# Optimization experiments

Hardware: AMD Instinct MI355X
Metric: run time of the kernel (lower is better)

Reference implementation:

```python
import jax, jax.numpy as jnp
import numpy as np

NUM_HEADS = 16
LORA_RANK = 64
LORA_ALPHA = 1.0


def setup_inputs() -> dict:
    key = jax.random.key(0)
    ks = jax.random.split(key, 9)
    B, N, C, r = 16, 1024, 1024, LORA_RANK
    s = lambda k, shp, sc=0.02: (jax.random.normal(k, shp, dtype=jnp.float32) * sc)
    return {
        "x": jax.random.normal(ks[0], (B, N, C), dtype=jnp.float32),
        "W_qkv": s(ks[1], (3 * C, C)),
        "b_qkv": s(ks[2], (3 * C,)),
        "lora_kA": s(ks[3], (r, C), 1.0 / np.sqrt(r)),
        "lora_kB": s(ks[4], (C, r)),
        "lora_vA": s(ks[5], (r, C), 1.0 / np.sqrt(r)),
        "lora_vB": s(ks[6], (C, r)),
        "W_proj": s(ks[7], (C, C)),
        "b_proj": s(ks[8], (C,)),
    }


def reference(x, W_qkv, b_qkv, lora_kA, lora_kB, lora_vA, lora_vB, W_proj, b_proj):
    B, N, C = x.shape
    H = NUM_HEADS
    D = C // H
    scale = D ** -0.5
    lora_scale = LORA_ALPHA / LORA_RANK

    # qkv projection: (B,N,3C)
    qkv = x @ W_qkv.T + b_qkv
    # LoRA deltas for k and v: x @ A.T @ B.T * (alpha/rank)
    k_lora = ((x @ lora_kA.T) @ lora_kB.T) * lora_scale  # (B,N,C)
    v_lora = ((x @ lora_vA.T) @ lora_vB.T) * lora_scale  # (B,N,C)

    qkv = qkv.reshape(B, N, 3, H, D).transpose(2, 0, 3, 1, 4)  # (3,B,H,N,D)
    q, k, v = qkv[0], qkv[1], qkv[2]
    k = k + k_lora.reshape(B, N, H, D).transpose(0, 2, 1, 3)
    v = v + v_lora.reshape(B, N, H, D).transpose(0, 2, 1, 3)

    attn = jnp.einsum('bhqd,bhkd->bhqk', q, k) * scale  # (B,H,N,N)
    attn = jax.nn.softmax(attn, axis=-1)
    out = jnp.einsum('bhqk,bhkd->bhqd', attn, v)  # (B,H,N,D)
    out = out.transpose(0, 2, 1, 3).reshape(B, N, C)
    return out @ W_proj.T + b_proj
```

## Files before the change

### kernel.cpp

```cpp
#include <hip/hip_runtime.h>
#include <hip/hip_bf16.h>
#include <stdint.h>

#define B_  16
#define N_  1024
#define C_  1024
#define H_  16
#define Dh  64
#define M_  (B_*N_)
#define QSCALE (0.125f * 1.44269504f)

typedef __attribute__((ext_vector_type(8)))  short short8;
typedef __attribute__((ext_vector_type(4)))  float f32x4;
typedef __attribute__((ext_vector_type(16))) float f32x16;

__device__ __forceinline__ ushort f2bf(float f) {
  union { float f; uint32_t u; } v; v.f = f;
  uint32_t u = v.u;
  u += 0x7fffu + ((u >> 16) & 1u);
  return (ushort)(u >> 16);
}

__device__ __forceinline__ ushort f2bf_fast(float f) {
  union { float f; uint32_t u; } v; v.f = f;
  return (ushort)((v.u + 0x8000u) >> 16);
}

__device__ __forceinline__ float exp2fast(float x) {
#if __has_builtin(__builtin_amdgcn_exp2f)
  return __builtin_amdgcn_exp2f(x);
#else
  return exp2f(x);
#endif
}

__device__ __forceinline__ void gload_lds16(const ushort* g, ushort* l) {
  __builtin_amdgcn_global_load_lds((const __attribute__((address_space(1))) void*)g,
                                   (__attribute__((address_space(3))) void*)l, 16, 0, 0);
}

struct CastSegs {
  const float* src[7];
  ushort*      dst[7];
  int          cum[7];
  float        scale[7];
};

__global__ void cast_all_k(CastSegs sg, int total4) {
  int i = blockIdx.x * blockDim.x + threadIdx.x;
  int stride = gridDim.x * blockDim.x;
  for (; i < total4; i += stride) {
    int s = 0;
    #pragma unroll
    for (int k = 0; k < 6; ++k) s += (i >= sg.cum[k]);
    int base = s ? sg.cum[s-1] : 0;
    int li = i - base;
    float sc = sg.scale[s];
    float4 v = reinterpret_cast<const float4*>(sg.src[s])[li];
    ushort4 o;
    o.x = f2bf(v.x * sc);
    o.y = f2bf(v.y * sc);
    o.z = f2bf(v.z * sc);
    o.w = f2bf(v.w * sc);
    reinterpret_cast<ushort4*>(sg.dst[s])[li] = o;
  }
}

template<int MODE>
__global__ __launch_bounds__(256)
void gemm128(const ushort* __restrict__ A, int lda,
             const ushort* __restrict__ Bm, int ldb,
             const float* __restrict__ bias,
             const ushort* __restrict__ A2,
             const ushort* __restrict__ B2k, const ushort* __restrict__ B2v,
             ushort* __restrict__ oq, ushort* __restrict__ ok, ushort* __restrict__ ov,
             float* __restrict__ of, int ldo)
{
  __shared__ ushort sA[2][128*32];
  __shared__ ushort sB[2][128*32];
  const int t = threadIdx.x;
  const int lane = t & 63, w = t >> 6;
  const int wr = w >> 1, wc = w & 1;
  const int r = lane & 15, g = lane >> 4;
  const int m0 = blockIdx.x * 128, n0 = blockIdx.y * 128;

  const int s = n0 >> 10;
  int nt = 32;
  const ushort* A2b = nullptr; const ushort* B2 = nullptr; int n0loc = 0;
  if (MODE == 1 && s == 1) {
    nt = 34;
    A2b = A2;
    B2 = B2k;
    n0loc = n0 - 1024;
  }
  if (MODE == 3) nt = 34;

  auto stage = [&](int buf, int tt) {
    const ushort* Ab; const ushort* Bb; int ldaT, ldbT;
    if (tt < 32) { Ab = A + m0*lda + tt*32; ldaT = lda; Bb = Bm + n0*ldb + tt*32; ldbT = ldb; }
    else if (MODE == 3) {
      Ab = A2 + m0*64 + (tt-32)*32; ldaT = 64;
      Bb = B2k + n0*128 + (tt-32)*32; ldbT = 128;
    } else {
      Ab = A2b + m0*128 + (tt-32)*32; ldaT = 128;
      Bb = B2 + n0loc*64 + (tt-32)*32; ldbT = 64;
    }
    #pragma unroll
    for (int i = 0; i < 2; ++i) {
      int c = i*256 + t;
      gload_lds16(Ab + (c>>2)*ldaT + (c&3)*8, &sA[buf][c*8]);
      gload_lds16(Bb + (c>>2)*ldbT + (c&3)*8, &sB[buf][c*8]);
    }
  };

  f32x4 acc[4][4];
  #pragma unroll
  for (int i=0;i<4;++i)
    #pragma unroll
    for (int j=0;j<4;++j) acc[i][j] = (f32x4){0.f,0.f,0.f,0.f};

  stage(0, 0);
  __syncthreads();
  for (int tt = 0; tt < nt; ++tt) {
    int cur = tt & 1;
    if (tt + 1 < nt) stage(cur ^ 1, tt + 1);
    short8 af[4], bfr[4];
    #pragma unroll
    for (int i=0;i<4;++i) af[i]  = *(const short8*)&sA[cur][(wr*64 + i*16 + r)*32 + g*8];
    #pragma unroll
    for (int j=0;j<4;++j) bfr[j] = *(const short8*)&sB[cur][(wc*64 + j*16 + r)*32 + g*8];
    #pragma unroll
    for (int i=0;i<4;++i)
      #pragma unroll
      for (int j=0;j<4;++j)
        acc[i][j] = __builtin_amdgcn_mfma_f32_16x16x32_bf16(af[i], bfr[j], acc[i][j], 0,0,0);
    __syncthreads();
  }

  #pragma unroll
  for (int i=0;i<4;++i) {
    #pragma unroll
    for (int j=0;j<4;++j) {
      #pragma unroll
      for (int rr=0;rr<4;++rr) {
        int m = m0 + wr*64 + i*16 + g*4 + rr;
        int n = n0 + wc*64 + j*16 + r;
        float v = acc[i][j][rr];
        if (MODE == 0) {
          oq[m*128 + n] = f2bf(v);
        } else if (MODE == 1) {
          v += bias[n];
          int b = m >> 10, nq = m & 1023;
          int c = n & 1023, h = c >> 6, d = c & 63;
          int idx = ((b*H_ + h)*N_ + nq)*Dh + d;
          if (s == 0)      oq[idx] = f2bf(v * QSCALE);
          else             ok[idx] = f2bf(v);
        } else if (MODE == 3) {
          v += bias[m];
          int h = m >> 6, d = m & 63;
          int b = n >> 10, nq = n & 1023;
          ov[((b*H_ + h)*Dh + d)*N_ + nq] = f2bf(v);
        } else {
          of[m*ldo + n] = v + bias[n];
        }
      }
    }
  }
}

__global__ __launch_bounds__(512)
void flash_attn32(const ushort* __restrict__ qb, const ushort* __restrict__ kb,
                  const ushort* __restrict__ vb, ushort* __restrict__ out)
{
  __shared__ ushort Kt[2][64*64];
  __shared__ ushort Vt[2][64*64];
  const int t = threadIdx.x, w = t >> 6, lane = t & 63;
  const int ql = lane & 31, hi = lane >> 5;

  int bid = (blockIdx.x & 7) * 128 + (blockIdx.x >> 3);
  const int bh = bid >> 2, qt = bid & 3;
  const int b = bh >> 4, h = bh & 15;
  const ushort* Q  = qb + bh * (N_*Dh);
  const ushort* K  = kb + bh * (N_*Dh);
  const ushort* VT = vb + bh * (Dh*N_);
  const int q0 = qt*256 + w*32;

  short8 qf[4];
  #pragma unroll
  for (int ds=0; ds<4; ++ds)
    qf[ds] = *(const short8*)&Q[(q0 + ql)*Dh + ds*16 + hi*8];

  short8 ones;
  #pragma unroll
  for (int j=0;j<8;++j) ones[j] = (short)0x3F80;

  f32x16 o0, o1, lacc;
  #pragma unroll
  for (int r=0;r<16;++r) { o0[r]=0.f; o1[r]=0.f; lacc[r]=0.f; }
  float m = -1e30f;

  const int srow = t >> 3, scc = (t & 7) ^ ((t >> 3) & 7);
  const ushort* Ksrc = K  + srow*Dh + scc*8;
  const ushort* Vsrc = VT + srow*N_ + scc*8;
  ushort* Kdst = &Kt[0][t*8];
  ushort* Vdst = &Vt[0][t*8];

  const int krA = ql, krB = 32 + ql;
  const int kbaseA = krA*64, kbaseB = krB*64, kmA = krA & 7, kmB = krB & 7;

  auto stage = [&](int buf, int kt) {
    gload_lds16(Ksrc + kt*(64*Dh), Kdst + buf*(64*64));
    gload_lds16(Vsrc + kt*64,      Vdst + buf*(64*64));
  };

  stage(0, 0);

  for (int kt = 0; kt < 16; ++kt) {
    int cur = kt & 1;
    asm volatile("s_waitcnt vmcnt(0)" ::: "memory");
    __builtin_amdgcn_sched_barrier(0);
    __builtin_amdgcn_s_barrier();
    if (kt < 15) stage(cur ^ 1, kt + 1);

    const ushort* Kl = &Kt[cur][0];
    const ushort* Vl = &Vt[cur][0];

    f32x16 s0, s1;
    #pragma unroll
    for (int r=0;r<16;++r) { s0[r]=0.f; s1[r]=0.f; }
    __builtin_amdgcn_s_setprio(1);
    #pragma unroll
    for (int ds=0; ds<4; ++ds) {
      int sc0 = ds*2 + hi;
      short8 kfA = *(const short8*)&Kl[kbaseA + ((sc0 ^ kmA)*8)];
      short8 kfB = *(const short8*)&Kl[kbaseB + ((sc0 ^ kmB)*8)];
      s0 = __builtin_amdgcn_mfma_f32_32x32x16_bf16(kfA, qf[ds], s0, 0,0,0);
      s1 = __builtin_amdgcn_mfma_f32_32x32x16_bf16(kfB, qf[ds], s1, 0,0,0);
    }
    __builtin_amdgcn_s_setprio(0);

    float pm = -1e30f;
    #pragma unroll
    for (int r=0;r<16;++r) pm = fmaxf(pm, fmaxf(s0[r], s1[r]));
    pm = fmaxf(pm, __shfl_xor(pm, 32));

    if (__any(pm > m + 8.f)) {
      float nm = fmaxf(m, pm);
      float fac = exp2fast(m - nm);
      m = nm;
      #pragma unroll
      for (int r=0;r<16;++r) {
        int qr = (r&3) + 8*(r>>2) + 4*hi;
        float facr = __shfl(fac, qr);
        o0[r] *= facr; o1[r] *= facr; lacc[r] *= facr;
      }
    }

    #pragma unroll
    for (int sg=0; sg<4; ++sg) {
      const int rb = (sg & 1) * 8;
      float e0,e1,e2,e3,e4,e5,e6,e7;
      if (sg < 2) {
        e0=exp2fast(s0[rb+0]-m); e1=exp2fast(s0[rb+1]-m);
        e2=exp2fast(s0[rb+2]-m); e3=exp2fast(s0[rb+3]-m);
        e4=exp2fast(s0[rb+4]-m); e5=exp2fast(s0[rb+5]-m);
        e6=exp2fast(s0[rb+6]-m); e7=exp2fast(s0[rb+7]-m);
      } else {
        e0=exp2fast(s1[rb+0]-m); e1=exp2fast(s1[rb+1]-m);
        e2=exp2fast(s1[rb+2]-m); e3=exp2fast(s1[rb+3]-m);
        e4=exp2fast(s1[rb+4]-m); e5=exp2fast(s1[rb+5]-m);
        e6=exp2fast(s1[rb+6]-m); e7=exp2fast(s1[rb+7]-m);
      }
      uint32_t w01 = (uint32_t)f2bf_fast(e0) | ((uint32_t)f2bf_fast(e1) << 16);
      uint32_t w23 = (uint32_t)f2bf_fast(e2) | ((uint32_t)f2bf_fast(e3) << 16);
      uint32_t w45 = (uint32_t)f2bf_fast(e4) | ((uint32_t)f2bf_fast(e5) << 16);
      uint32_t w67 = (uint32_t)f2bf_fast(e6) | ((uint32_t)f2bf_fast(e7) << 16);
      uint32_t x01 = __shfl_xor(w01, 32);
      uint32_t x23 = __shfl_xor(w23, 32);
      uint32_t x45 = __shfl_xor(w45, 32);
      uint32_t x67 = __shfl_xor(w67, 32);
      union { uint32_t u[4]; short8 s8; } pu;
      pu.u[0] = hi ? x45 : w01;
      pu.u[1] = hi ? x67 : w23;
      pu.u[2] = hi ? w45 : x01;
      pu.u[3] = hi ? w67 : x23;
      short8 pf = pu.s8;

      int sc0 = sg*2 + hi;
      short8 vfA = *(const short8*)&Vl[kbaseA + ((sc0 ^ kmA)*8)];
      short8 vfB = *(const short8*)&Vl[kbaseB + ((sc0 ^ kmB)*8)];
      __builtin_amdgcn_s_setprio(1);
      o0   = __builtin_amdgcn_mfma_f32_32x32x16_bf16(pf, vfA, o0, 0,0,0);
      o1   = __builtin_amdgcn_mfma_f32_32x32x16_bf16(pf, vfB, o1, 0,0,0);
      lacc = __builtin_amdgcn_mfma_f32_32x32x16_bf16(pf, ones, lacc, 0,0,0);
      __builtin_amdgcn_s_setprio(0);
    }
  }

  #pragma unroll
  for (int r=0;r<16;++r) {
    float inv = 1.f / lacc[r];
    int qr = (r&3) + 8*(r>>2) + 4*hi;
    int row = b*N_ + q0 + qr;
    out[row*C_ + h*Dh + ql]      = f2bf(o0[r] * inv);
    out[row*C_ + h*Dh + 32 + ql] = f2bf(o1[r] * inv);
  }
}

extern "C" void kernel_launch(void* const* d_in, const int* in_sizes, int n_in,
                              void* d_out, int out_size, void* d_ws, size_t ws_size,
                              hipStream_t stream)
{
  const float* x      = (const float*)d_in[0];
  const float* W_qkv  = (const float*)d_in[1];
  const float* b_qkv  = (const float*)d_in[2];
  const float* kA     = (const float*)d_in[3];
  const float* kB     = (const float*)d_in[4];
  const float* vA     = (const float*)d_in[5];
  const float* vB     = (const float*)d_in[6];
  const float* W_proj = (const float*)d_in[7];
  const float* b_proj = (const float*)d_in[8];
  float* out = (float*)d_out;

  ushort* ws    = (ushort*)d_ws;
  ushort* xb    = ws;
  ushort* wqkvb = xb + 16777216;
  ushort* kvAb  = wqkvb + 3145728;
  ushort* kBb   = kvAb + 131072;
  ushort* vBb   = kBb + 65536;
  ushort* wprojb= vBb + 65536;
  ushort* tkv   = wprojb + 1048576;
  ushort* qbuf  = tkv + 2097152;
  ushort* kbuf  = qbuf + 16777216;
  ushort* vbuf  = kbuf + 16777216;
  ushort* attn  = xb;

  const float ls = 1.0f / 64.0f;

  CastSegs sg;
  const float* srcs[7] = { x, W_qkv, kA, vA, kB, vB, W_proj };
  ushort* dsts[7]      = { xb, wqkvb, kvAb, kvAb + 65536, kBb, vBb, wprojb };
  int     n4s[7]       = { 16777216/4, 3145728/4, 65536/4, 65536/4, 65536/4, 65536/4, 1048576/4 };
  float   scs[7]       = { 1.f, 1.f, 1.f, 1.f, ls, ls, 1.f };
  int cum = 0;
  for (int i = 0; i < 7; ++i) {
    sg.src[i] = srcs[i]; sg.dst[i] = dsts[i]; sg.scale[i] = scs[i];
    cum += n4s[i]; sg.cum[i] = cum;
  }
  cast_all_k<<<dim3(4096), dim3(256), 0, stream>>>(sg, cum);

  gemm128<0><<<dim3(128, 1), dim3(256), 0, stream>>>(
      xb, 1024, kvAb, 1024, nullptr, nullptr, nullptr, nullptr,
      tkv, nullptr, nullptr, nullptr, 0);

  gemm128<1><<<dim3(128, 16), dim3(256), 0, stream>>>(
      xb, 1024, wqkvb, 1024, b_qkv, tkv, kBb, nullptr,
      qbuf, kbuf, nullptr, nullptr, 0);

  gemm128<3><<<dim3(8, 128), dim3(256), 0, stream>>>(
      wqkvb + 2048*1024, 1024, xb, 1024, b_qkv + 2048, vBb, tkv + 64, nullptr,
      nullptr, nullptr, vbuf, nullptr, 0);

  flash_attn32<<<dim3(1024), dim3(512), 0, stream>>>(qbuf, kbuf, vbuf, attn);

  gemm128<2><<<dim3(128, 8), dim3(256), 0, stream>>>(
      attn, 1024, wprojb, 1024, b_proj, nullptr, nullptr, nullptr,
      nullptr, nullptr, nullptr, out, 1024);
}
```

Measured before the change: 394.0 us.

## Drop ones-MFMA row-sum in flash attention and use 256-thread blocks

Replaces the extra MFMA against a ones vector, which accumulated the softmax denominator, with a scalar fp32 running sum of the exponentials that is combined across half-waves at the end. This removes one of three MFMAs in the PV loop along with a 16-register accumulator. The attention kernel also moves from 512-thread to 256-thread blocks (2048 blocks, 128 queries each, launch_bounds 256,4), with each thread staging two K/V chunks per tile. The row max is computed as a tree reduction. Smaller blocks raise occupancy and shorten barriers, but each block reloads K/V tiles for fewer queries, doubling K/V traffic.

```diff
diff --git a/kernel.cpp b/kernel.cpp
--- a/kernel.cpp
+++ b/kernel.cpp
@@ -168,7 +168,7 @@
   }
 }
 
-__global__ __launch_bounds__(512)
+__global__ __launch_bounds__(256, 4)
 void flash_attn32(const ushort* __restrict__ qb, const ushort* __restrict__ kb,
                   const ushort* __restrict__ vb, ushort* __restrict__ out)
 {
@@ -177,40 +177,41 @@
   const int t = threadIdx.x, w = t >> 6, lane = t & 63;
   const int ql = lane & 31, hi = lane >> 5;
 
-  int bid = (blockIdx.x & 7) * 128 + (blockIdx.x >> 3);
-  const int bh = bid >> 2, qt = bid & 3;
+  int bid = (blockIdx.x & 7) * 256 + (blockIdx.x >> 3);
+  const int bh = bid >> 3, qt = bid & 7;
   const int b = bh >> 4, h = bh & 15;
   const ushort* Q  = qb + bh * (N_*Dh);
   const ushort* K  = kb + bh * (N_*Dh);
   const ushort* VT = vb + bh * (Dh*N_);
-  const int q0 = qt*256 + w*32;
+  const int q0 = qt*128 + w*32;
 
   short8 qf[4];
   #pragma unroll
   for (int ds=0; ds<4; ++ds)
     qf[ds] = *(const short8*)&Q[(q0 + ql)*Dh + ds*16 + hi*8];
 
-  short8 ones;
-  #pragma unroll
-  for (int j=0;j<8;++j) ones[j] = (short)0x3F80;
-
-  f32x16 o0, o1, lacc;
-  #pragma unroll
-  for (int r=0;r<16;++r) { o0[r]=0.f; o1[r]=0.f; lacc[r]=0.f; }
+  f32x16 o0, o1;
+  #pragma unroll
+  for (int r=0;r<16;++r) { o0[r]=0.f; o1[r]=0.f; }
+  float lsum = 0.f;
   float m = -1e30f;
 
   const int srow = t >> 3, scc = (t & 7) ^ ((t >> 3) & 7);
-  const ushort* Ksrc = K  + srow*Dh + scc*8;
-  const ushort* Vsrc = VT + srow*N_ + scc*8;
+  const ushort* Ksrc0 = K  + srow*Dh + scc*8;
+  const ushort* Vsrc0 = VT + srow*N_ + scc*8;
   ushort* Kdst = &Kt[0][t*8];
   ushort* Vdst = &Vt[0][t*8];
 
-  const int krA = ql, krB = 32 + ql;
-  const int kbaseA = krA*64, kbaseB = krB*64, kmA = krA & 7, kmB = krB & 7;
+  const int kbaseA = ql*64, kbaseB = (32 + ql)*64;
+  const int kmA = ql & 7, kmB = kmA;
 
   auto stage = [&](int buf, int kt) {
-    gload_lds16(Ksrc + kt*(64*Dh), Kdst + buf*(64*64));
-    gload_lds16(Vsrc + kt*64,      Vdst + buf*(64*64));
+    const ushort* Kp = Ksrc0 + kt*(64*Dh);
+    const ushort* Vp = Vsrc0 + kt*64;
+    gload_lds16(Kp,          Kdst + buf*4096);
+    gload_lds16(Kp + 32*Dh,  Kdst + buf*4096 + 2048);
+    gload_lds16(Vp,          Vdst + buf*4096);
+    gload_lds16(Vp + 32*N_,  Vdst + buf*4096 + 2048);
   };
 
   stage(0, 0);
@@ -239,20 +240,25 @@
     }
     __builtin_amdgcn_s_setprio(0);
 
-    float pm = -1e30f;
-    #pragma unroll
-    for (int r=0;r<16;++r) pm = fmaxf(pm, fmaxf(s0[r], s1[r]));
+    float tm[8];
+    #pragma unroll
+    for (int i=0;i<8;++i)
+      tm[i] = fmaxf(fmaxf(s0[i], s0[i+8]), fmaxf(s1[i], s1[i+8]));
+    float ta = fmaxf(fmaxf(tm[0],tm[1]), fmaxf(tm[2],tm[3]));
+    float tb = fmaxf(fmaxf(tm[4],tm[5]), fmaxf(tm[6],tm[7]));
+    float pm = fmaxf(ta, tb);
     pm = fmaxf(pm, __shfl_xor(pm, 32));
 
     if (__any(pm > m + 8.f)) {
       float nm = fmaxf(m, pm);
       float fac = exp2fast(m - nm);
       m = nm;
+      lsum *= fac;
       #pragma unroll
       for (int r=0;r<16;++r) {
         int qr = (r&3) + 8*(r>>2) + 4*hi;
         float facr = __shfl(fac, qr);
-        o0[r] *= facr; o1[r] *= facr; lacc[r] *= facr;
+        o0[r] *= facr; o1[r] *= facr;
       }
     }
 
@@ -271,6 +277,7 @@
         e4=exp2fast(s1[rb+4]-m); e5=exp2fast(s1[rb+5]-m);
         e6=exp2fast(s1[rb+6]-m); e7=exp2fast(s1[rb+7]-m);
       }
+      lsum += ((e0+e1)+(e2+e3)) + ((e4+e5)+(e6+e7));
       uint32_t w01 = (uint32_t)f2bf_fast(e0) | ((uint32_t)f2bf_fast(e1) << 16);
       uint32_t w23 = (uint32_t)f2bf_fast(e2) | ((uint32_t)f2bf_fast(e3) << 16);
       uint32_t w45 = (uint32_t)f2bf_fast(e4) | ((uint32_t)f2bf_fast(e5) << 16);
@@ -290,20 +297,21 @@
       short8 vfA = *(const short8*)&Vl[kbaseA + ((sc0 ^ kmA)*8)];
       short8 vfB = *(const short8*)&Vl[kbaseB + ((sc0 ^ kmB)*8)];
       __builtin_amdgcn_s_setprio(1);
-      o0   = __builtin_amdgcn_mfma_f32_32x32x16_bf16(pf, vfA, o0, 0,0,0);
-      o1   = __builtin_amdgcn_mfma_f32_32x32x16_bf16(pf, vfB, o1, 0,0,0);
-      lacc = __builtin_amdgcn_mfma_f32_32x32x16_bf16(pf, ones, lacc, 0,0,0);
+      o0 = __builtin_amdgcn_mfma_f32_32x32x16_bf16(pf, vfA, o0, 0,0,0);
+      o1 = __builtin_amdgcn_mfma_f32_32x32x16_bf16(pf, vfB, o1, 0,0,0);
       __builtin_amdgcn_s_setprio(0);
     }
   }
 
+  float lfull = lsum + __shfl_xor(lsum, 32);
+  float inv = 1.f / lfull;
   #pragma unroll
   for (int r=0;r<16;++r) {
-    float inv = 1.f / lacc[r];
     int qr = (r&3) + 8*(r>>2) + 4*hi;
+    float invr = __shfl(inv, qr);
     int row = b*N_ + q0 + qr;
-    out[row*C_ + h*Dh + ql]      = f2bf(o0[r] * inv);
-    out[row*C_ + h*Dh + 32 + ql] = f2bf(o1[r] * inv);
+    out[row*C_ + h*Dh + ql]      = f2bf(o0[r] * invr);
+    out[row*C_ + h*Dh + 32 + ql] = f2bf(o1[r] * invr);
   }
 }
 
@@ -361,7 +369,7 @@
       wqkvb + 2048*1024, 1024, xb, 1024, b_qkv + 2048, vBb, tkv + 64, nullptr,
       nullptr, nullptr, vbuf, nullptr, 0);
 
-  flash_attn32<<<dim3(1024), dim3(512), 0, stream>>>(qbuf, kbuf, vbuf, attn);
+  flash_attn32<<<dim3(2048), dim3(256), 0, stream>>>(qbuf, kbuf, vbuf, attn);
 
   gemm128<2><<<dim3(128, 8), dim3(256), 0, stream>>>(
       attn, 1024, wprojb, 1024, b_proj, nullptr, nullptr, nullptr,
```

New measurement: 363.4 us. 1.08x faster.
